# Kernel tuning notes

Measured on AMD Instinct MI355X. Metric: run time of the kernel, lower is better.

Reference implementation:

```python
import jax, jax.numpy as jnp
import numpy as np

K = 3
PAD = 1
EPS = 1e-5


def _conv2d(x, w, b):
    y = jax.lax.conv_general_dilated(x, w, window_strides=(1, 1), padding='SAME',
                                     dimension_numbers=('NCHW', 'OIHW', 'NCHW'))
    return y + b[None, :, None, None]


def _bn(x, g, beta, m, v):
    inv = jax.lax.rsqrt(v + EPS)
    return (x - m[None, :, None, None]) * (g * inv)[None, :, None, None] + beta[None, :, None, None]


def _deform_conv2d(x, offset, w, b):
    # torchvision deform_conv2d (v1, no mask), stride=1, pad=1, 3x3 kernel.
    B, Cin, H, W = x.shape
    Cout = w.shape[0]
    # offset: [B, 2*K*K, H, W] -> (dy, dx) per kernel tap
    off = offset.reshape(B, K * K, 2, H, W)
    dy, dx = off[:, :, 0], off[:, :, 1]                     # [B, K2, H, W]
    ii, jj = jnp.meshgrid(jnp.arange(K), jnp.arange(K), indexing='ij')
    ki = (ii.reshape(-1) - PAD).astype(x.dtype)             # [K2]
    kj = (jj.reshape(-1) - PAD).astype(x.dtype)
    py = jnp.arange(H, dtype=x.dtype)[None, None, :, None] + ki[None, :, None, None] + dy
    px = jnp.arange(W, dtype=x.dtype)[None, None, None, :] + kj[None, :, None, None] + dx
    y0 = jnp.floor(py)
    x0 = jnp.floor(px)
    wy = py - y0
    wx = px - x0
    flat = x.reshape(B, Cin, H * W)

    def gather(yc, xc):
        valid = ((yc >= 0) & (yc < H) & (xc >= 0) & (xc < W)).astype(x.dtype)
        yi = jnp.clip(yc, 0, H - 1).astype(jnp.int32)
        xi = jnp.clip(xc, 0, W - 1).astype(jnp.int32)
        idx = (yi * W + xi).reshape(B, -1)                  # [B, K2*H*W]
        g = jax.vmap(lambda f, i: f[:, i])(flat, idx)       # [B, Cin, K2*H*W]
        return g.reshape(B, Cin, K * K, H, W) * valid[:, None]

    v = (gather(y0,     x0    ) * ((1 - wy) * (1 - wx))[:, None]
         + gather(y0,     x0 + 1) * ((1 - wy) * wx)[:, None]
         + gather(y0 + 1, x0    ) * (wy * (1 - wx))[:, None]
         + gather(y0 + 1, x0 + 1) * (wy * wx)[:, None])     # [B, Cin, K2, H, W]
    out = jnp.einsum('bckhw,ock->bohw', v, w.reshape(Cout, Cin, K * K))
    return out + b[None, :, None, None]


def setup_inputs() -> dict:
    key = jax.random.key(0)
    ks = jax.random.split(key, 12)
    d = {}
    d['x'] = jax.random.normal(ks[0], (32, 3, 64, 64), jnp.float32)
    d['offset1_w'] = jax.random.normal(ks[1], (18, 3, 3, 3), jnp.float32) * 0.05
    d['offset1_b'] = jnp.zeros((18,), jnp.float32)
    d['conv1_w'] = jax.random.normal(ks[2], (64, 3, 3, 3), jnp.float32) * 0.1
    d['conv1_b'] = jnp.zeros((64,), jnp.float32)
    d['bn1_gamma'] = jnp.ones((64,), jnp.float32)
    d['bn1_beta'] = jnp.zeros((64,), jnp.float32)
    d['bn1_mean'] = jnp.zeros((64,), jnp.float32)
    d['bn1_var'] = jax.random.uniform(ks[3], (64,), jnp.float32, 0.5, 1.5)
    d['offset2_w'] = jax.random.normal(ks[4], (18, 64, 3, 3), jnp.float32) * 0.02
    d['offset2_b'] = jnp.zeros((18,), jnp.float32)
    d['conv2_w'] = jax.random.normal(ks[5], (128, 64, 3, 3), jnp.float32) * 0.05
    d['conv2_b'] = jnp.zeros((128,), jnp.float32)
    d['bn2_gamma'] = jnp.ones((128,), jnp.float32)
    d['bn2_beta'] = jnp.zeros((128,), jnp.float32)
    d['bn2_mean'] = jnp.zeros((128,), jnp.float32)
    d['bn2_var'] = jax.random.uniform(ks[6], (128,), jnp.float32, 0.5, 1.5)
    d['fc1_w'] = jax.random.normal(ks[7], (256, 128), jnp.float32) * 0.08
    d['fc1_b'] = jnp.zeros((256,), jnp.float32)
    d['fc2_w'] = jax.random.normal(ks[8], (200, 256), jnp.float32) * 0.06
    d['fc2_b'] = jnp.zeros((200,), jnp.float32)
    return d


def reference(x, offset1_w, offset1_b, conv1_w, conv1_b, bn1_gamma, bn1_beta, bn1_mean, bn1_var,
              offset2_w, offset2_b, conv2_w, conv2_b, bn2_gamma, bn2_beta, bn2_mean, bn2_var,
              fc1_w, fc1_b, fc2_w, fc2_b):
    # Eval-mode forward (dropout layers are identity / deterministic).
    off1 = _conv2d(x, offset1_w, offset1_b)
    h = _deform_conv2d(x, off1, conv1_w, conv1_b)
    h = jax.nn.relu(_bn(h, bn1_gamma, bn1_beta, bn1_mean, bn1_var))
    off2 = _conv2d(h, offset2_w, offset2_b)
    h = _deform_conv2d(h, off2, conv2_w, conv2_b)
    h = jax.nn.relu(_bn(h, bn2_gamma, bn2_beta, bn2_mean, bn2_var))
    h = h.mean(axis=(2, 3))                                 # global avg pool -> [B, 128]
    h = jax.nn.relu(h @ fc1_w.T + fc1_b)
    return h @ fc2_w.T + fc2_b
```

## Files before the change

### kernel.cpp

```cpp
#include <hip/hip_runtime.h>

#define EPS 1e-5f

#define W1OT 0
#define W1B  1024
#define W2T  4096
#define W2OB 40960
#define SC1  59392
#define SH1  59456
#define SC2  59520
#define SH2  59648
#define POOL 59776
#define XP   65536
#define H1B  589824
#define W1B_U   2048
#define W2T_U   8192
#define W2OB_U  81920
#define H1B_U   1179648

typedef __attribute__((ext_vector_type(8))) short bhalf8;
typedef __attribute__((ext_vector_type(8))) unsigned short u16x8;
typedef __attribute__((ext_vector_type(4))) float f32x4;
typedef __attribute__((ext_vector_type(4))) uint u32x4;

#define APAD 40

struct Tap { int i00, i01, i10, i11; float w00, w01, w10, w11; };

__device__ __forceinline__ Tap make_tap(float py, float px) {
    float y0f = floorf(py), x0f = floorf(px);
    float wy = py - y0f, wx = px - x0f;
    bool by0 = (y0f >= 0.f)  && (y0f < 64.f);
    bool by1 = (y0f >= -1.f) && (y0f < 63.f);
    bool bx0 = (x0f >= 0.f)  && (x0f < 64.f);
    bool bx1 = (x0f >= -1.f) && (x0f < 63.f);
    int y0 = min(max((int)y0f, 0), 63);
    int y1 = min(max((int)y0f + 1, 0), 63);
    int x0 = min(max((int)x0f, 0), 63);
    int x1 = min(max((int)x0f + 1, 0), 63);
    Tap tp;
    tp.i00 = y0 * 64 + x0; tp.i01 = y0 * 64 + x1;
    tp.i10 = y1 * 64 + x0; tp.i11 = y1 * 64 + x1;
    tp.w00 = (by0 && bx0) ? (1.f - wy) * (1.f - wx) : 0.f;
    tp.w01 = (by0 && bx1) ? (1.f - wy) * wx         : 0.f;
    tp.w10 = (by1 && bx0) ? wy * (1.f - wx)         : 0.f;
    tp.w11 = (by1 && bx1) ? wy * wx                 : 0.f;
    return tp;
}

__device__ __forceinline__ ushort f2bf(float f) {
    union { float f; uint u; } a; a.f = f;
    uint u = a.u;
    return (ushort)((u + 0x7fffu + ((u >> 16) & 1u)) >> 16);
}
__device__ __forceinline__ float bf2f(ushort u) {
    union { uint u; float f; } a; a.u = ((uint)u) << 16;
    return a.f;
}

__device__ __forceinline__ uint cvtpk_bf16(float a, float b) {
    uint r;
    asm("v_cvt_pk_bf16_f32 %0, %1, %2" : "=v"(r) : "v"(a), "v"(b));
    return r;
}

__device__ __forceinline__ f32x4 evenf(uint4 u) {
    union { uint u; float f; } a;
    f32x4 r;
    a.u = u.x << 16; r[0] = a.f;
    a.u = u.y << 16; r[1] = a.f;
    a.u = u.z << 16; r[2] = a.f;
    a.u = u.w << 16; r[3] = a.f;
    return r;
}
__device__ __forceinline__ f32x4 oddf(uint4 u) {
    union { uint u; float f; } a;
    f32x4 r;
    a.u = u.x & 0xffff0000u; r[0] = a.f;
    a.u = u.y & 0xffff0000u; r[1] = a.f;
    a.u = u.z & 0xffff0000u; r[2] = a.f;
    a.u = u.w & 0xffff0000u; r[3] = a.f;
    return r;
}

__device__ __forceinline__ void gl_lds16(const void* g, void* l) {
    __builtin_amdgcn_global_load_lds(
        (const __attribute__((address_space(1))) unsigned int*)g,
        (__attribute__((address_space(3))) unsigned int*)l, 16, 0, 0);
}

__global__ __launch_bounds__(256) void k_prep(
    const float* __restrict__ x,
    const float* __restrict__ o1w, const float* __restrict__ c1w,
    const float* __restrict__ o2w, const float* __restrict__ c2w,
    const float* __restrict__ c1b, const float* __restrict__ g1,
    const float* __restrict__ be1, const float* __restrict__ m1,
    const float* __restrict__ v1,
    const float* __restrict__ c2b, const float* __restrict__ g2,
    const float* __restrict__ be2, const float* __restrict__ m2,
    const float* __restrict__ v2,
    float* __restrict__ ws) {
    int tid = blockIdx.x * 256 + threadIdx.x;
    ushort* wsu = (ushort*)ws;
    if (tid < 648) {
        int co = tid % 18, tc = tid / 18, c = tc & 3, t = tc >> 2;
        ws[W1OT + tid] = (c < 3) ? o1w[(co * 3 + c) * 9 + t] : 0.f;
    } else if (tid < 2696) {
        int i = tid - 648;
        int n = i >> 5, k = i & 31;
        float v = 0.f;
        if (k < 27) { int c = k % 3, t = k / 3; v = c1w[(n * 3 + c) * 9 + t]; }
        wsu[W1B_U + i] = f2bf(v);
    } else if (tid < 76424) {
        int i = tid - 2696;
        int c = i & 63, n = (i >> 6) & 127, t = i >> 13;
        wsu[W2T_U + i] = f2bf(c2w[(n * 64 + c) * 9 + t]);
    } else if (tid < 94856) {
        int i = tid - 76424;
        int j = i & 7, r = (i >> 3) & 15, q = (i >> 7) & 3;
        int nt = (i >> 9) & 1, ks = (i >> 10) & 1, t = i >> 11;
        int n = nt * 16 + r;
        int c = ks * 32 + q * 8 + j;
        float v = (n < 18) ? o2w[(n * 64 + c) * 9 + t] : 0.f;
        wsu[W2OB_U + i] = f2bf(v);
    } else if (tid < 94920) {
        int i = tid - 94856;
        float s = g1[i] * rsqrtf(v1[i] + EPS);
        ws[SC1 + i] = s;
        ws[SH1 + i] = (c1b[i] - m1[i]) * s + be1[i];
    } else if (tid < 95048) {
        int i = tid - 94920;
        float s = g2[i] * rsqrtf(v2[i] + EPS);
        ws[SC2 + i] = s;
        ws[SH2 + i] = (c2b[i] - m2[i]) * s + be2[i];
    } else if (tid < 99144) {
        ws[POOL + tid - 95048] = 0.f;
    } else if (tid < 230216) {
        int i = tid - 99144;
        int b = i >> 12, hw = i & 4095;
        const float* xpp = x + (size_t)b * 3 * 4096 + hw;
        f32x4 o;
        o[0] = xpp[0]; o[1] = xpp[4096]; o[2] = xpp[8192]; o[3] = 0.f;
        *(f32x4*)(ws + XP + (size_t)i * 4) = o;
    }
}

__global__ __launch_bounds__(256, 4) void k_def1(
    const float* __restrict__ o1b, float* __restrict__ ws) {
    __shared__ ushort Alds[256 * APAD];
    __shared__ ushort Blds[64 * APAD];
    __shared__ float wo[648];
    __shared__ float scl[128];
    int tid = threadIdx.x;
    for (int i = tid; i < 648; i += 256) wo[i] = ws[W1OT + i];
    if (tid < 128) scl[tid] = ws[SC1 + tid];
    {
        const ushort* src = (const ushort*)ws + W1B_U;
        if (tid < 128) {
            int n = tid >> 1, half = (tid & 1) * 16;
            *(uint4*)(Blds + n * APAD + half)     = *(const uint4*)(src + n * 32 + half);
            *(uint4*)(Blds + n * APAD + half + 8) = *(const uint4*)(src + n * 32 + half + 8);
        }
    }
    int g = blockIdx.x;
    int b = (g & 7) * 4 + ((g >> 3) & 3);
    int row0 = (g >> 5) * 4;
    int h = row0 + (tid >> 6), w = tid & 63;
    const float* xp = ws + XP + (size_t)b * 16384;

    float off[18];
#pragma unroll
    for (int i = 0; i < 18; ++i) off[i] = o1b[i];
    __syncthreads();
#pragma unroll
    for (int t = 0; t < 9; ++t) {
        int yy = h + t / 3 - 1, xx = w + t % 3 - 1;
        f32x4 pv = (f32x4)0.f;
        if (yy >= 0 && yy < 64 && xx >= 0 && xx < 64)
            pv = *(const f32x4*)(xp + (yy * 64 + xx) * 4);
#pragma unroll
        for (int c = 0; c < 3; ++c) {
            const float* wp = wo + (t * 4 + c) * 18;
#pragma unroll
            for (int co = 0; co < 18; ++co) off[co] += pv[c] * wp[co];
        }
    }
    ushort ob[32];
#pragma unroll
    for (int i = 0; i < 32; ++i) ob[i] = 0;
#pragma unroll
    for (int t = 0; t < 9; ++t) {
        Tap tp = make_tap((float)(h + t / 3 - 1) + off[2 * t],
                          (float)(w + t % 3 - 1) + off[2 * t + 1]);
        f32x4 c00 = *(const f32x4*)(xp + tp.i00 * 4);
        f32x4 c01 = *(const f32x4*)(xp + tp.i01 * 4);
        f32x4 c10 = *(const f32x4*)(xp + tp.i10 * 4);
        f32x4 c11 = *(const f32x4*)(xp + tp.i11 * 4);
        f32x4 vt = tp.w00 * c00 + tp.w01 * c01 + tp.w10 * c10 + tp.w11 * c11;
        ob[t * 3 + 0] = f2bf(vt[0]);
        ob[t * 3 + 1] = f2bf(vt[1]);
        ob[t * 3 + 2] = f2bf(vt[2]);
    }
    {
        ushort* ar = Alds + tid * APAD;
#pragma unroll
        for (int i = 0; i < 4; ++i)
            *(uint4*)(ar + i * 8) = *(const uint4*)(ob + i * 8);
    }
    __syncthreads();

    int lane = tid & 63, wv = tid >> 6;
    int r = lane & 15, q = lane >> 4;
    bhalf8 bf[4];
#pragma unroll
    for (int nt = 0; nt < 4; ++nt)
        bf[nt] = *(const bhalf8*)(Blds + (nt * 16 + r) * APAD + q * 8);
    f32x4 acc[4][4];
#pragma unroll
    for (int mt = 0; mt < 4; ++mt) {
        bhalf8 af = *(const bhalf8*)(Alds + (wv * 64 + mt * 16 + r) * APAD + q * 8);
#pragma unroll
        for (int nt = 0; nt < 4; ++nt)
            acc[mt][nt] = __builtin_amdgcn_mfma_f32_16x16x32_bf16(af, bf[nt], (f32x4)0.f, 0, 0, 0);
    }
    ushort* hb = (ushort*)ws + H1B_U + (size_t)(b * 4096 + row0 * 64) * 64;
#pragma unroll
    for (int nt = 0; nt < 4; ++nt) {
        int col = nt * 16 + r;
        float s0 = scl[col], s1 = scl[64 + col];
#pragma unroll
        for (int mt = 0; mt < 4; ++mt) {
            int pxl = wv * 64 + mt * 16 + q * 4;
#pragma unroll
            for (int rr = 0; rr < 4; ++rr)
                hb[(size_t)(pxl + rr) * 64 + col] =
                    f2bf(fmaxf(acc[mt][nt][rr] * s0 + s1, 0.f));
        }
    }
}

__global__ __launch_bounds__(256, 5) void k_def2(
    const float* __restrict__ o2b, float* __restrict__ ws) {
    __shared__ __align__(16) char smem[20992];
    ushort* Bd  = (ushort*)smem;
    float* offL = (float*)(smem + 16384);
    int g = blockIdx.x;
    int b = (g & 7) * 4 + ((g >> 3) & 3);
    int row = g >> 5;
    int tid = threadIdx.x, lane = tid & 63, wv = tid >> 6;
    int r = lane & 15, q = lane >> 4;
    int px = wv * 16 + r;
    const ushort* hb = (const ushort*)ws + H1B_U + (size_t)b * 262144;
    const ushort* wB = (const ushort*)ws + W2T_U;
    const ushort* btl = (const ushort*)ws + W2OB_U + lane * 8;
    int sOff[4];
#pragma unroll
    for (int i = 0; i < 4; ++i) {
        int lin = wv * 4096 + i * 1024 + lane * 16;
        sOff[i] = lin ^ (((lin >> 7) & 7) << 4);
    }

    f32x4 acc2[2];
    acc2[0] = (f32x4)0.f; acc2[1] = (f32x4)0.f;
#pragma unroll
    for (int t = 0; t < 9; ++t) {
        int yy = row + t / 3 - 1;
        int xx = px + t % 3 - 1;
        bool val = (yy >= 0 && yy < 64 && xx >= 0 && xx < 64);
        int yyc = min(max(yy, 0), 63), xxc = min(max(xx, 0), 63);
        const ushort* ap = hb + (size_t)(yyc * 64 + xxc) * 64 + q * 8;
#pragma unroll
        for (int ks = 0; ks < 2; ++ks) {
            bhalf8 af = val ? *(const bhalf8*)(ap + ks * 32) : (bhalf8)(short)0;
#pragma unroll
            for (int nt = 0; nt < 2; ++nt) {
                bhalf8 bf = *(const bhalf8*)(btl + (size_t)((t * 2 + ks) * 2 + nt) * 512);
                acc2[nt] = __builtin_amdgcn_mfma_f32_16x16x32_bf16(af, bf, acc2[nt], 0, 0, 0);
            }
        }
    }
#pragma unroll
    for (int nt = 0; nt < 2; ++nt) {
        int n = nt * 16 + r;
        if (n < 18) {
            float bias = o2b[n];
#pragma unroll
            for (int rr = 0; rr < 4; ++rr)
                offL[(wv * 16 + q * 4 + rr) * 18 + n] = acc2[nt][rr] + bias;
        }
    }
    __syncthreads();

    f32x4 acc[8];
#pragma unroll
    for (int j = 0; j < 8; ++j) acc[j] = (f32x4)0.f;

    for (int t = 0; t < 9; ++t) {
        if (t) __syncthreads();
        float oy = offL[px * 18 + 2 * t];
        float ox = offL[px * 18 + 2 * t + 1];
        Tap tp = make_tap((float)(row + t / 3 - 1) + oy,
                          (float)(px + t % 3 - 1) + ox);
        int o00 = tp.i00 * 64 + q * 8;
        int o01 = tp.i01 * 64 + q * 8;
        int o10 = tp.i10 * 64 + q * 8;
        int o11 = tp.i11 * 64 + q * 8;
        uint4 a00 = *(const uint4*)(hb + o00);
        uint4 a01 = *(const uint4*)(hb + o01);
        uint4 a10 = *(const uint4*)(hb + o10);
        uint4 a11 = *(const uint4*)(hb + o11);
        {
            const char* wsrc = (const char*)wB + t * 16384;
#pragma unroll
            for (int i = 0; i < 4; ++i)
                gl_lds16(wsrc + sOff[i], smem + wv * 4096 + i * 1024);
        }
        bhalf8 af0;
        {
            f32x4 ve = tp.w00 * evenf(a00) + tp.w01 * evenf(a01)
                     + tp.w10 * evenf(a10) + tp.w11 * evenf(a11);
            f32x4 vo = tp.w00 * oddf(a00) + tp.w01 * oddf(a01)
                     + tp.w10 * oddf(a10) + tp.w11 * oddf(a11);
            uint c0 = cvtpk_bf16(ve[0], vo[0]);
            uint c1 = cvtpk_bf16(ve[1], vo[1]);
            uint c2 = cvtpk_bf16(ve[2], vo[2]);
            uint c3 = cvtpk_bf16(ve[3], vo[3]);
            u32x4 uu; uu[0] = c0; uu[1] = c1; uu[2] = c2; uu[3] = c3;
            af0 = __builtin_bit_cast(bhalf8, uu);
        }
        bhalf8 af1;
        {
            uint4 b00 = *(const uint4*)(hb + o00 + 32);
            uint4 b01 = *(const uint4*)(hb + o01 + 32);
            uint4 b10 = *(const uint4*)(hb + o10 + 32);
            uint4 b11 = *(const uint4*)(hb + o11 + 32);
            f32x4 ve = tp.w00 * evenf(b00) + tp.w01 * evenf(b01)
                     + tp.w10 * evenf(b10) + tp.w11 * evenf(b11);
            f32x4 vo = tp.w00 * oddf(b00) + tp.w01 * oddf(b01)
                     + tp.w10 * oddf(b10) + tp.w11 * oddf(b11);
            uint c0 = cvtpk_bf16(ve[0], vo[0]);
            uint c1 = cvtpk_bf16(ve[1], vo[1]);
            uint c2 = cvtpk_bf16(ve[2], vo[2]);
            uint c3 = cvtpk_bf16(ve[3], vo[3]);
            u32x4 uu; uu[0] = c0; uu[1] = c1; uu[2] = c2; uu[3] = c3;
            af1 = __builtin_bit_cast(bhalf8, uu);
        }
        __syncthreads();
#pragma unroll
        for (int nt = 0; nt < 8; ++nt) {
            int us = ((nt * 16 + r) * 64 + q * 8) ^ ((r & 7) << 3);
            bhalf8 bf = *(const bhalf8*)(Bd + us);
            acc[nt] = __builtin_amdgcn_mfma_f32_16x16x32_bf16(af0, bf, acc[nt], 0, 0, 0);
        }
#pragma unroll
        for (int nt = 0; nt < 8; ++nt) {
            int us = ((nt * 16 + r) * 64 + 32 + q * 8) ^ ((r & 7) << 3);
            bhalf8 bf = *(const bhalf8*)(Bd + us);
            acc[nt] = __builtin_amdgcn_mfma_f32_16x16x32_bf16(af1, bf, acc[nt], 0, 0, 0);
        }
    }
    const float* sc = ws + SC2;
    const float* sh = ws + SH2;
    float* pool = ws + POOL;
#pragma unroll
    for (int nt = 0; nt < 8; ++nt) {
        int col = nt * 16 + r;
        float s0 = sc[col], s1 = sh[col];
        float s = 0.f;
#pragma unroll
        for (int rr = 0; rr < 4; ++rr)
            s += fmaxf(acc[nt][rr] * s0 + s1, 0.f);
        s += __shfl_xor(s, 16);
        s += __shfl_xor(s, 32);
        if (lane < 16) atomicAdd(&pool[b * 128 + col], s);
    }
}

__global__ __launch_bounds__(256) void k_fc(
    const float* __restrict__ w1, const float* __restrict__ b1,
    const float* __restrict__ w2, const float* __restrict__ b2,
    const float* __restrict__ ws, float* __restrict__ out) {
    int b = blockIdx.x, o = threadIdx.x;
    __shared__ float pl[128];
    __shared__ float hl[256];
    if (o < 128) pl[o] = ws[POOL + b * 128 + o] * (1.f / 4096.f);
    __syncthreads();
    float s = b1[o];
    const float* wp = w1 + o * 128;
#pragma unroll 8
    for (int c = 0; c < 128; ++c) s += pl[c] * wp[c];
    hl[o] = fmaxf(s, 0.f);
    __syncthreads();
    if (o < 200) {
        float s2 = b2[o];
        const float* wp2 = w2 + o * 256;
#pragma unroll 8
        for (int c = 0; c < 256; ++c) s2 += hl[c] * wp2[c];
        out[b * 200 + o] = s2;
    }
}

extern "C" void kernel_launch(void* const* d_in, const int* in_sizes, int n_in,
                              void* d_out, int out_size, void* d_ws, size_t ws_size,
                              hipStream_t stream) {
    const float* x   = (const float*)d_in[0];
    const float* o1w = (const float*)d_in[1];
    const float* o1b = (const float*)d_in[2];
    const float* c1w = (const float*)d_in[3];
    const float* c1b = (const float*)d_in[4];
    const float* g1  = (const float*)d_in[5];
    const float* be1 = (const float*)d_in[6];
    const float* m1  = (const float*)d_in[7];
    const float* v1  = (const float*)d_in[8];
    const float* o2w = (const float*)d_in[9];
    const float* o2b = (const float*)d_in[10];
    const float* c2w = (const float*)d_in[11];
    const float* c2b = (const float*)d_in[12];
    const float* g2  = (const float*)d_in[13];
    const float* be2 = (const float*)d_in[14];
    const float* m2  = (const float*)d_in[15];
    const float* v2  = (const float*)d_in[16];
    const float* f1w = (const float*)d_in[17];
    const float* f1b = (const float*)d_in[18];
    const float* f2w = (const float*)d_in[19];
    const float* f2b = (const float*)d_in[20];
    float* ws  = (float*)d_ws;
    float* out = (float*)d_out;

    k_prep<<<900, 256, 0, stream>>>(x, o1w, c1w, o2w, c2w,
                                    c1b, g1, be1, m1, v1,
                                    c2b, g2, be2, m2, v2, ws);
    k_def1<<<512, 256, 0, stream>>>(o1b, ws);
    k_def2<<<2048, 256, 0, stream>>>(o2b, ws);
    k_fc<<<32, 256, 0, stream>>>(f1w, f1b, f2w, f2b, ws, out);
}
```

Measured before the change: 297.5 us.

## Double-buffer weight tiles and prefetch next-tap gathers in second deformable conv

```diff
diff --git a/kernel.cpp b/kernel.cpp
--- a/kernel.cpp
+++ b/kernel.cpp
@@ -239,11 +239,10 @@
     }
 }
 
-__global__ __launch_bounds__(256, 5) void k_def2(
+__global__ __launch_bounds__(256, 4) void k_def2(
     const float* __restrict__ o2b, float* __restrict__ ws) {
-    __shared__ __align__(16) char smem[20992];
-    ushort* Bd  = (ushort*)smem;
-    float* offL = (float*)(smem + 16384);
+    __shared__ __align__(16) char smem[37376];
+    float* offL = (float*)(smem + 32768);
     int g = blockIdx.x;
     int b = (g & 7) * 4 + ((g >> 3) & 3);
     int row = g >> 5;
@@ -259,6 +258,9 @@
         int lin = wv * 4096 + i * 1024 + lane * 16;
         sOff[i] = lin ^ (((lin >> 7) & 7) << 4);
     }
+#pragma unroll
+    for (int i = 0; i < 4; ++i)
+        gl_lds16((const char*)wB + sOff[i], smem + wv * 4096 + i * 1024);
 
     f32x4 acc2[2];
     acc2[0] = (f32x4)0.f; acc2[1] = (f32x4)0.f;
@@ -295,68 +297,100 @@
 #pragma unroll
     for (int j = 0; j < 8; ++j) acc[j] = (f32x4)0.f;
 
+    Tap tp[2];
+    uint4 gq[2][8];
+    {
+        float oy = offL[px * 18 + 0];
+        float ox = offL[px * 18 + 1];
+        tp[0] = make_tap((float)(row - 1) + oy, (float)(px - 1) + ox);
+        int o00 = tp[0].i00 * 64 + q * 8;
+        int o01 = tp[0].i01 * 64 + q * 8;
+        int o10 = tp[0].i10 * 64 + q * 8;
+        int o11 = tp[0].i11 * 64 + q * 8;
+        gq[0][0] = *(const uint4*)(hb + o00);
+        gq[0][1] = *(const uint4*)(hb + o01);
+        gq[0][2] = *(const uint4*)(hb + o10);
+        gq[0][3] = *(const uint4*)(hb + o11);
+        gq[0][4] = *(const uint4*)(hb + o00 + 32);
+        gq[0][5] = *(const uint4*)(hb + o01 + 32);
+        gq[0][6] = *(const uint4*)(hb + o10 + 32);
+        gq[0][7] = *(const uint4*)(hb + o11 + 32);
+    }
+
+#pragma unroll
     for (int t = 0; t < 9; ++t) {
-        if (t) __syncthreads();
-        float oy = offL[px * 18 + 2 * t];
-        float ox = offL[px * 18 + 2 * t + 1];
-        Tap tp = make_tap((float)(row + t / 3 - 1) + oy,
-                          (float)(px + t % 3 - 1) + ox);
-        int o00 = tp.i00 * 64 + q * 8;
-        int o01 = tp.i01 * 64 + q * 8;
-        int o10 = tp.i10 * 64 + q * 8;
-        int o11 = tp.i11 * 64 + q * 8;
-        uint4 a00 = *(const uint4*)(hb + o00);
-        uint4 a01 = *(const uint4*)(hb + o01);
-        uint4 a10 = *(const uint4*)(hb + o10);
-        uint4 a11 = *(const uint4*)(hb + o11);
+        const int cur = t & 1, nxt = (t + 1) & 1;
+        if (t < 8) {
+            const char* wsrc = (const char*)wB + (t + 1) * 16384;
+            char* dst = smem + nxt * 16384 + wv * 4096;
+#pragma unroll
+            for (int i = 0; i < 4; ++i)
+                gl_lds16(wsrc + sOff[i], dst + i * 1024);
+            float oy = offL[px * 18 + 2 * (t + 1)];
+            float ox = offL[px * 18 + 2 * (t + 1) + 1];
+            tp[nxt] = make_tap((float)(row + (t + 1) / 3 - 1) + oy,
+                               (float)(px + (t + 1) % 3 - 1) + ox);
+            int o00 = tp[nxt].i00 * 64 + q * 8;
+            int o01 = tp[nxt].i01 * 64 + q * 8;
+            int o10 = tp[nxt].i10 * 64 + q * 8;
+            int o11 = tp[nxt].i11 * 64 + q * 8;
+            gq[nxt][0] = *(const uint4*)(hb + o00);
+            gq[nxt][1] = *(const uint4*)(hb + o01);
+            gq[nxt][2] = *(const uint4*)(hb + o10);
+            gq[nxt][3] = *(const uint4*)(hb + o11);
+            gq[nxt][4] = *(const uint4*)(hb + o00 + 32);
+            gq[nxt][5] = *(const uint4*)(hb + o01 + 32);
+            gq[nxt][6] = *(const uint4*)(hb + o10 + 32);
+            gq[nxt][7] = *(const uint4*)(hb + o11 + 32);
+        }
+        float w00 = tp[cur].w00, w01 = tp[cur].w01;
+        float w10 = tp[cur].w10, w11 = tp[cur].w11;
+        bhalf8 af0, af1;
         {
-            const char* wsrc = (const char*)wB + t * 16384;
-#pragma unroll
-            for (int i = 0; i < 4; ++i)
-                gl_lds16(wsrc + sOff[i], smem + wv * 4096 + i * 1024);
-        }
-        bhalf8 af0;
+            f32x4 ve = w00 * evenf(gq[cur][0]) + w01 * evenf(gq[cur][1])
+                     + w10 * evenf(gq[cur][2]) + w11 * evenf(gq[cur][3]);
+            f32x4 vo = w00 * oddf(gq[cur][0]) + w01 * oddf(gq[cur][1])
+                     + w10 * oddf(gq[cur][2]) + w11 * oddf(gq[cur][3]);
+            u32x4 uu;
+            uu[0] = cvtpk_bf16(ve[0], vo[0]);
+            uu[1] = cvtpk_bf16(ve[1], vo[1]);
+            uu[2] = cvtpk_bf16(ve[2], vo[2]);
+            uu[3] = cvtpk_bf16(ve[3], vo[3]);
+            af0 = __builtin_bit_cast(bhalf8, uu);
+        }
         {
-            f32x4 ve = tp.w00 * evenf(a00) + tp.w01 * evenf(a01)
-                     + tp.w10 * evenf(a10) + tp.w11 * evenf(a11);
-            f32x4 vo = tp.w00 * oddf(a00) + tp.w01 * oddf(a01)
-                     + tp.w10 * oddf(a10) + tp.w11 * oddf(a11);
-            uint c0 = cvtpk_bf16(ve[0], vo[0]);
-            uint c1 = cvtpk_bf16(ve[1], vo[1]);
-            uint c2 = cvtpk_bf16(ve[2], vo[2]);
-            uint c3 = cvtpk_bf16(ve[3], vo[3]);
-            u32x4 uu; uu[0] = c0; uu[1] = c1; uu[2] = c2; uu[3] = c3;
-            af0 = __builtin_bit_cast(bhalf8, uu);
-        }
-        bhalf8 af1;
-        {
-            uint4 b00 = *(const uint4*)(hb + o00 + 32);
-            uint4 b01 = *(const uint4*)(hb + o01 + 32);
-            uint4 b10 = *(const uint4*)(hb + o10 + 32);
-            uint4 b11 = *(const uint4*)(hb + o11 + 32);
-            f32x4 ve = tp.w00 * evenf(b00) + tp.w01 * evenf(b01)
-                     + tp.w10 * evenf(b10) + tp.w11 * evenf(b11);
-            f32x4 vo = tp.w00 * oddf(b00) + tp.w01 * oddf(b01)
-                     + tp.w10 * oddf(b10) + tp.w11 * oddf(b11);
-            uint c0 = cvtpk_bf16(ve[0], vo[0]);
-            uint c1 = cvtpk_bf16(ve[1], vo[1]);
-            uint c2 = cvtpk_bf16(ve[2], vo[2]);
-            uint c3 = cvtpk_bf16(ve[3], vo[3]);
-            u32x4 uu; uu[0] = c0; uu[1] = c1; uu[2] = c2; uu[3] = c3;
+            f32x4 ve = w00 * evenf(gq[cur][4]) + w01 * evenf(gq[cur][5])
+                     + w10 * evenf(gq[cur][6]) + w11 * evenf(gq[cur][7]);
+            f32x4 vo = w00 * oddf(gq[cur][4]) + w01 * oddf(gq[cur][5])
+                     + w10 * oddf(gq[cur][6]) + w11 * oddf(gq[cur][7]);
+            u32x4 uu;
+            uu[0] = cvtpk_bf16(ve[0], vo[0]);
+            uu[1] = cvtpk_bf16(ve[1], vo[1]);
+            uu[2] = cvtpk_bf16(ve[2], vo[2]);
+            uu[3] = cvtpk_bf16(ve[3], vo[3]);
             af1 = __builtin_bit_cast(bhalf8, uu);
         }
-        __syncthreads();
+        __builtin_amdgcn_sched_barrier(0);
+        asm volatile("s_waitcnt vmcnt(12)" ::: "memory");
+        __builtin_amdgcn_s_barrier();
+        __builtin_amdgcn_sched_barrier(0);
+        const ushort* Bq = (const ushort*)(smem + cur * 16384);
 #pragma unroll
         for (int nt = 0; nt < 8; ++nt) {
             int us = ((nt * 16 + r) * 64 + q * 8) ^ ((r & 7) << 3);
-            bhalf8 bf = *(const bhalf8*)(Bd + us);
+            bhalf8 bf = *(const bhalf8*)(Bq + us);
             acc[nt] = __builtin_amdgcn_mfma_f32_16x16x32_bf16(af0, bf, acc[nt], 0, 0, 0);
         }
 #pragma unroll
         for (int nt = 0; nt < 8; ++nt) {
             int us = ((nt * 16 + r) * 64 + 32 + q * 8) ^ ((r & 7) << 3);
-            bhalf8 bf = *(const bhalf8*)(Bd + us);
+            bhalf8 bf = *(const bhalf8*)(Bq + us);
             acc[nt] = __builtin_amdgcn_mfma_f32_16x16x32_bf16(af1, bf, acc[nt], 0, 0, 0);
+        }
+        if (t < 8) {
+            __builtin_amdgcn_sched_barrier(0);
+            __builtin_amdgcn_s_barrier();
+            __builtin_amdgcn_sched_barrier(0);
         }
     }
     const float* sc = ws + SC2;
```

After: 288.7 us. 3.0% less time.
